# Kernel tuning notes

Measured on AMD Instinct MI355X. Metric: run time of the kernel, lower is better.

## Reference

```python
import jax, jax.numpy as jnp
import numpy as np

EPS = 1e-6

def _rms_norm(x, w):
    # per-head RMSNorm over last dim (head_dim)
    var = jnp.mean(jnp.square(x), axis=-1, keepdims=True)
    return x * jax.lax.rsqrt(var + EPS) * w

def _linear(x, w, b):
    # torch nn.Linear: y = x @ W^T + b
    return jnp.einsum('bsd,od->bso', x, w) + b

def setup_inputs() -> dict:
    key = jax.random.key(0)
    ks = jax.random.split(key, 16)
    B, S, S_enc, D, H, HD = 1, 2048, 256, 1536, 24, 64
    w = lambda k: jax.random.normal(k, (D, D), dtype=jnp.float32) * 0.02
    return {
        'hidden_states': jax.random.normal(ks[0], (B, S, D), dtype=jnp.float32),
        'encoder_hidden_states': jax.random.normal(ks[1], (B, S_enc, D), dtype=jnp.float32),
        'attention_mask': jnp.zeros((B, 1, 1, S + S_enc), dtype=jnp.float32),
        'to_q_weight': w(ks[2]), 'to_q_bias': jnp.zeros((D,), jnp.float32),
        'to_k_weight': w(ks[3]), 'to_k_bias': jnp.zeros((D,), jnp.float32),
        'to_v_weight': w(ks[4]), 'to_v_bias': jnp.zeros((D,), jnp.float32),
        'norm_q_weight': jnp.ones((HD,), jnp.float32),
        'norm_k_weight': jnp.ones((HD,), jnp.float32),
        'add_q_proj_weight': w(ks[5]), 'add_q_proj_bias': jnp.zeros((D,), jnp.float32),
        'add_k_proj_weight': w(ks[6]), 'add_k_proj_bias': jnp.zeros((D,), jnp.float32),
        'add_v_proj_weight': w(ks[7]), 'add_v_proj_bias': jnp.zeros((D,), jnp.float32),
        'norm_added_q_weight': jnp.ones((HD,), jnp.float32),
        'norm_added_k_weight': jnp.ones((HD,), jnp.float32),
        'to_out_0_weight': w(ks[8]), 'to_out_0_bias': jnp.zeros((D,), jnp.float32),
        'to_add_out_weight': w(ks[9]), 'to_add_out_bias': jnp.zeros((D,), jnp.float32),
        'attn_heads': 24,
        'attn_head_dim': 64,
    }

def reference(hidden_states, encoder_hidden_states, attention_mask,
              to_q_weight, to_q_bias, to_k_weight, to_k_bias, to_v_weight, to_v_bias,
              norm_q_weight, norm_k_weight,
              add_q_proj_weight, add_q_proj_bias, add_k_proj_weight, add_k_proj_bias,
              add_v_proj_weight, add_v_proj_bias,
              norm_added_q_weight, norm_added_k_weight,
              to_out_0_weight, to_out_0_bias, to_add_out_weight, to_add_out_bias,
              attn_heads, attn_head_dim):
    B, S, D = hidden_states.shape
    S_enc = encoder_hidden_states.shape[1]
    H, HD = attn_heads, attn_head_dim
    scale = float(HD) ** -0.5

    def split_heads(x):  # [B,T,H*HD] -> [B,H,T,HD]
        return x.reshape(B, -1, H, HD).transpose(0, 2, 1, 3)

    # hidden-stream QKV + per-head RMSNorm on q,k
    q = _rms_norm(split_heads(_linear(hidden_states, to_q_weight, to_q_bias)), norm_q_weight)
    k = _rms_norm(split_heads(_linear(hidden_states, to_k_weight, to_k_bias)), norm_k_weight)
    v = split_heads(_linear(hidden_states, to_v_weight, to_v_bias))

    # encoder-stream QKV + per-head RMSNorm on q,k
    eq = _rms_norm(split_heads(_linear(encoder_hidden_states, add_q_proj_weight, add_q_proj_bias)), norm_added_q_weight)
    ek = _rms_norm(split_heads(_linear(encoder_hidden_states, add_k_proj_weight, add_k_proj_bias)), norm_added_k_weight)
    ev = split_heads(_linear(encoder_hidden_states, add_v_proj_weight, add_v_proj_bias))

    # concat streams along sequence: [B,H,S+S_enc,HD]
    q = jnp.concatenate([q, eq], axis=2)
    k = jnp.concatenate([k, ek], axis=2)
    v = jnp.concatenate([v, ev], axis=2)

    # SDPA with additive mask
    scores = jnp.einsum('bhqd,bhkd->bhqk', q, k) * scale + attention_mask
    probs = jax.nn.softmax(scores, axis=-1)
    out = jnp.einsum('bhqk,bhkd->bhqd', probs, v)  # [B,H,T,HD]
    out = out.transpose(0, 2, 1, 3).reshape(B, S + S_enc, H * HD)

    # split back into image / text streams, separate output projections
    attn_output = _linear(out[:, :S], to_out_0_weight, to_out_0_bias)
    context_attn_output = _linear(out[:, S:], to_add_out_weight, to_add_out_bias)
    del context_attn_output  # AttentionFunc returns only the hidden-stream output
    return attn_output
```

## Files before the change

### kernel.cpp

```cpp
#include <hip/hip_runtime.h>
#include <cstdint>


typedef __attribute__((ext_vector_type(8))) short s16x8;
typedef __attribute__((ext_vector_type(4))) float f32x4;

#define LOG2E 1.4426950408889634f

__device__ __forceinline__ short f2bf(float f) {
  union { float f; uint32_t u; } v; v.f = f;
  uint32_t r = v.u + 0x7FFFu + ((v.u >> 16) & 1u);
  return (short)(r >> 16);
}
__device__ __forceinline__ short f2bf_fast(float f) {
  union { float f; uint32_t u; } v; v.f = f;
  return (short)((v.u + 0x8000u) >> 16);
}

typedef uint32_t __attribute__((address_space(1)))* gas_u32;
typedef uint32_t __attribute__((address_space(3)))* las_u32;

__device__ __forceinline__ void gload_lds16(const short* g, short* l) {
  __builtin_amdgcn_global_load_lds((gas_u32)(g), (las_u32)(l), 16, 0, 0);
}

struct CvtSeg { const float* src; short* dst; int n4; };
struct CvtArgs { CvtSeg s[8]; };

__global__ __launch_bounds__(256) void cvt_bf16_kernel(CvtArgs a) {
  const int stride = gridDim.x * blockDim.x;
  const int tid = blockIdx.x * blockDim.x + threadIdx.x;
  for (int i = 0; i < 8; ++i) {
    const float4* src = (const float4*)a.s[i].src;
    short* dst = a.s[i].dst;
    const int n4 = a.s[i].n4;
    for (int j = tid; j < n4; j += stride) {
      float4 v = src[j];
      short4 o;
      o.x = f2bf(v.x); o.y = f2bf(v.y); o.z = f2bf(v.z); o.w = f2bf(v.w);
      *(short4*)(dst + (size_t)j * 4) = o;
    }
  }
}

enum { MODE_Q = 0, MODE_K = 1, MODE_V = 2, MODE_OUT = 3 };

struct GemmCfg {
  const short* A;
  const short* W;
  const float* bias;
  const float* normw;
  void* dst;
  int toff;
  int mode;
  int mtiles;
};
struct GemmArgs { GemmCfg c[5]; };

__global__ __launch_bounds__(256) void proj_gemm_kernel(GemmArgs args) {
  const GemmCfg cfg = args.c[blockIdx.z];
  if ((int)blockIdx.y >= cfg.mtiles) return;
  constexpr int K = 1536;
  __shared__ short As[8192];
  __shared__ short Bs[8192];
  const int t = threadIdx.x;
  const int lane = t & 63;
  const int wave = t >> 6;
  const int l16 = lane & 15;
  const int quad = lane >> 4;
  const int wm = wave >> 1;
  const int wn = wave & 1;

  const short* __restrict__ Ag = cfg.A + (size_t)(blockIdx.y * 128) * K;
  const short* __restrict__ Wg = cfg.W + (size_t)(blockIdx.x * 128) * K;
  const int srow = t >> 3;
  const int cpos = t & 7;
  const int srcc = cpos ^ (srow & 7);

  const f32x4 z4 = {0.f, 0.f, 0.f, 0.f};
  f32x4 acc[4][4];
#pragma unroll
  for (int i = 0; i < 4; ++i) {
#pragma unroll
    for (int j = 0; j < 4; ++j) acc[i][j] = z4;
  }

  for (int k0 = 0; k0 < K; k0 += 64) {
#pragma unroll
    for (int j = 0; j < 4; ++j) {
      const size_t roff = (size_t)(j * 32 + srow) * K + k0 + srcc * 8;
      gload_lds16(Ag + roff, As + j * 2048 + t * 8);
      gload_lds16(Wg + roff, Bs + j * 2048 + t * 8);
    }
    __syncthreads();
#pragma unroll
    for (int kh = 0; kh < 2; ++kh) {
      s16x8 af[4], bfr[4];
#pragma unroll
      for (int i = 0; i < 4; ++i) {
        int pos = (kh * 4 + quad) ^ (l16 & 7);
        af[i]  = *(const s16x8*)(As + (wm * 64 + i * 16 + l16) * 64 + pos * 8);
        bfr[i] = *(const s16x8*)(Bs + (wn * 64 + i * 16 + l16) * 64 + pos * 8);
      }
#pragma unroll
      for (int mi = 0; mi < 4; ++mi) {
#pragma unroll
        for (int ni = 0; ni < 4; ++ni)
          acc[mi][ni] = __builtin_amdgcn_mfma_f32_16x16x32_bf16(af[mi], bfr[ni], acc[mi][ni], 0, 0, 0);
      }
    }
    __syncthreads();
  }

  const int nbase = blockIdx.x * 128 + wn * 64;
  const int mbase = blockIdx.y * 128 + wm * 64;
  const int mode = cfg.mode;
  const int h = nbase >> 6;

  float biasv[4], nwv[4];
#pragma unroll
  for (int ni = 0; ni < 4; ++ni) {
    int col = nbase + ni * 16 + l16;
    biasv[ni] = cfg.bias[col];
    nwv[ni] = (mode == MODE_Q || mode == MODE_K) ? cfg.normw[col & 63] : 0.f;
  }

#pragma unroll
  for (int mi = 0; mi < 4; ++mi) {
    float vv[4][4];
#pragma unroll
    for (int ni = 0; ni < 4; ++ni) {
#pragma unroll
      for (int r = 0; r < 4; ++r) vv[ni][r] = acc[mi][ni][r] + biasv[ni];
    }
    if (mode == MODE_Q || mode == MODE_K) {
      float ss[4];
#pragma unroll
      for (int r = 0; r < 4; ++r)
        ss[r] = vv[0][r] * vv[0][r] + vv[1][r] * vv[1][r] +
                vv[2][r] * vv[2][r] + vv[3][r] * vv[3][r];
#pragma unroll
      for (int r = 0; r < 4; ++r) {
        ss[r] += __shfl_xor(ss[r], 1);
        ss[r] += __shfl_xor(ss[r], 2);
        ss[r] += __shfl_xor(ss[r], 4);
        ss[r] += __shfl_xor(ss[r], 8);
        float rs = rsqrtf(ss[r] * (1.0f / 64.0f) + 1e-6f);
#pragma unroll
        for (int ni = 0; ni < 4; ++ni) vv[ni][r] *= rs * nwv[ni];
      }
    }
    const int row0 = mbase + mi * 16 + quad * 4;
    if (mode == MODE_Q) {
      short* Qd = (short*)cfg.dst;
#pragma unroll
      for (int ni = 0; ni < 4; ++ni) {
        int d = ni * 16 + l16;
#pragma unroll
        for (int r = 0; r < 4; ++r)
          Qd[((size_t)h * 2048 + row0 + r) * 64 + d] = f2bf(vv[ni][r]);
      }
    } else if (mode == MODE_K) {
      short* Kd = (short*)cfg.dst;
#pragma unroll
      for (int ni = 0; ni < 4; ++ni) {
        int d = ni * 16 + l16;
#pragma unroll
        for (int r = 0; r < 4; ++r)
          Kd[((size_t)h * 2304 + cfg.toff + row0 + r) * 64 + d] = f2bf(vv[ni][r]);
      }
    } else if (mode == MODE_V) {
      short* Vd = (short*)cfg.dst;
#pragma unroll
      for (int ni = 0; ni < 4; ++ni) {
        int d = ni * 16 + l16;
        short4 o4;
        o4.x = f2bf(vv[ni][0]); o4.y = f2bf(vv[ni][1]);
        o4.z = f2bf(vv[ni][2]); o4.w = f2bf(vv[ni][3]);
        *(short4*)(Vd + ((size_t)h * 64 + d) * 2304 + cfg.toff + row0) = o4;
      }
    } else {
      float* Od = (float*)cfg.dst;
#pragma unroll
      for (int ni = 0; ni < 4; ++ni) {
        int col = nbase + ni * 16 + l16;
#pragma unroll
        for (int r = 0; r < 4; ++r)
          Od[(size_t)(row0 + r) * 1536 + col] = vv[ni][r];
      }
    }
  }
}

__global__ __launch_bounds__(256) void flash_kernel(
    const short* __restrict__ Q, const short* __restrict__ Kc,
    const short* __restrict__ VT, const float* __restrict__ mask,
    short* __restrict__ AO) {
  const int b = blockIdx.x;
  const int h = (b & 7) * 3 + ((b >> 3) % 3);
  const int q0 = ((b >> 3) / 3) * 32;
  const int lane = threadIdx.x & 63;
  const int wave = threadIdx.x >> 6;
  const int qw = wave & 1;
  const int ks = wave >> 1;
  const int l16 = lane & 15;
  const int quad = lane >> 4;

  __shared__ __align__(16) short smem[18432];
  short* Pw = smem + 16384 + wave * 512;

  const short* Kh = Kc + (size_t)h * 2304 * 64;
  const short* Vh = VT + (size_t)h * 64 * 2304;

  const short* Qrow = Q + ((size_t)h * 2048 + q0 + qw * 16 + l16) * 64;
  s16x8 aq0 = *(const s16x8*)(Qrow + quad * 8);
  s16x8 aq1 = *(const s16x8*)(Qrow + quad * 8 + 32);

  s16x8 ones;
#pragma unroll
  for (int i = 0; i < 8; ++i) ones[i] = (short)0x3F80;

  const f32x4 z4 = {0.f, 0.f, 0.f, 0.f};
  f32x4 o[4] = {z4, z4, z4, z4};
  f32x4 lacc = z4;
  const float SC = 0.125f * LOG2E;
  const int kbase = ks * 1152;

  auto stage = [&](int it, int buf) {
    const int kb = kbase + it * 32;
    short* kt = smem + (ks * 2 + buf) * 2048;
    short* vt = smem + 8192 + (ks * 2 + buf) * 2048;
#pragma unroll
    for (int c = 0; c < 2; ++c) {
      int s = c * 128 + qw * 64 + lane;
      int trow = s >> 3, cp = s & 7;
      gload_lds16(Kh + (size_t)(kb + trow) * 64 + (cp ^ (trow & 7)) * 8,
                  kt + c * 1024 + qw * 512 + lane * 8);
      int d = s >> 2, cpv = s & 3;
      gload_lds16(Vh + (size_t)d * 2304 + kb + ((cpv ^ ((d >> 1) & 3)) * 8),
                  vt + c * 1024 + qw * 512 + lane * 8);
    }
  };

  stage(0, 0);
  __syncthreads();

  for (int it = 0; it < 36; ++it) {
    const int buf = it & 1;
    if (it < 35) stage(it + 1, buf ^ 1);
    const short* kt = smem + (ks * 2 + buf) * 2048;
    const short* vt = smem + 8192 + (ks * 2 + buf) * 2048;
    const int kb = kbase + it * 32;

#pragma unroll
    for (int ni = 0; ni < 2; ++ni) {
      const int tt = ni * 16 + l16;
      const short* kr = kt + tt * 64;
      s16x8 bk0 = *(const s16x8*)(kr + ((quad ^ (tt & 7)) << 3));
      s16x8 bk1 = *(const s16x8*)(kr + (((quad + 4) ^ (tt & 7)) << 3));
      f32x4 p0 = __builtin_amdgcn_mfma_f32_16x16x32_bf16(aq0, bk0, z4, 0, 0, 0);
      f32x4 s  = __builtin_amdgcn_mfma_f32_16x16x32_bf16(aq1, bk1, p0, 0, 0, 0);
      float mvl = mask[kb + tt] * LOG2E;
      const int cc = tt >> 3;
#pragma unroll
      for (int rr = 0; rr < 4; ++rr) {
        float pv = __builtin_amdgcn_exp2f(fmaf(s[rr], SC, mvl));
        int prow = quad * 4 + rr;
        Pw[prow * 32 + ((cc ^ ((prow >> 1) & 3)) << 3) + (tt & 7)] = f2bf_fast(pv);
      }
    }
    s16x8 ap = *(const s16x8*)(Pw + l16 * 32 + ((quad ^ ((l16 >> 1) & 3)) << 3));
    lacc = __builtin_amdgcn_mfma_f32_16x16x32_bf16(ap, ones, lacc, 0, 0, 0);
#pragma unroll
    for (int ni = 0; ni < 4; ++ni) {
      const int d = ni * 16 + l16;
      s16x8 bv = *(const s16x8*)(vt + d * 32 + ((quad ^ ((d >> 1) & 3)) << 3));
      o[ni] = __builtin_amdgcn_mfma_f32_16x16x32_bf16(ap, bv, o[ni], 0, 0, 0);
    }
    __syncthreads();
  }

  f32x4* R = (f32x4*)smem;
  if (ks == 1) {
    f32x4* Rw = R + (qw * 64 + lane) * 5;
#pragma unroll
    for (int ni = 0; ni < 4; ++ni) Rw[ni] = o[ni];
    Rw[4] = lacc;
  }
  __syncthreads();
  if (ks == 0) {
    const f32x4* Rw = R + (qw * 64 + lane) * 5;
#pragma unroll
    for (int ni = 0; ni < 4; ++ni) o[ni] += Rw[ni];
    lacc += Rw[4];
#pragma unroll
    for (int rr = 0; rr < 4; ++rr) {
      float inv = 1.0f / lacc[rr];
      int tq = q0 + qw * 16 + quad * 4 + rr;
#pragma unroll
      for (int ni = 0; ni < 4; ++ni)
        AO[(size_t)tq * 1536 + h * 64 + ni * 16 + l16] = f2bf(o[ni][rr] * inv);
    }
  }
}

extern "C" void kernel_launch(void* const* d_in, const int* in_sizes, int n_in,
                              void* d_out, int out_size, void* d_ws, size_t ws_size,
                              hipStream_t stream) {
  (void)in_sizes; (void)n_in; (void)out_size; (void)ws_size;
  const float* hidden = (const float*)d_in[0];
  const float* enc    = (const float*)d_in[1];
  const float* amask  = (const float*)d_in[2];
  const float* wq  = (const float*)d_in[3];  const float* bq  = (const float*)d_in[4];
  const float* wk  = (const float*)d_in[5];  const float* bk  = (const float*)d_in[6];
  const float* wv  = (const float*)d_in[7];  const float* bv  = (const float*)d_in[8];
  const float* nqw = (const float*)d_in[9];  const float* nkw = (const float*)d_in[10];
  const float* wak = (const float*)d_in[13]; const float* bak = (const float*)d_in[14];
  const float* wav = (const float*)d_in[15]; const float* bav = (const float*)d_in[16];
  const float* nakw = (const float*)d_in[18];
  const float* wo  = (const float*)d_in[19]; const float* bo  = (const float*)d_in[20];
  float* out = (float*)d_out;

  char* p = (char*)d_ws;
  auto carve = [&](size_t bytes) { char* r = p; p += (bytes + 255) & ~(size_t)255; return r; };
  short* Xb   = (short*)carve((size_t)2048 * 1536 * 2);
  short* Eb   = (short*)carve((size_t)256 * 1536 * 2);
  short* Wqb  = (short*)carve((size_t)1536 * 1536 * 2);
  short* Wkb  = (short*)carve((size_t)1536 * 1536 * 2);
  short* Wvb  = (short*)carve((size_t)1536 * 1536 * 2);
  short* Wakb = (short*)carve((size_t)1536 * 1536 * 2);
  short* Wavb = (short*)carve((size_t)1536 * 1536 * 2);
  short* Wob  = (short*)carve((size_t)1536 * 1536 * 2);
  short* Qb   = (short*)carve((size_t)24 * 2048 * 64 * 2);
  short* Kb   = (short*)carve((size_t)24 * 2304 * 64 * 2);
  short* VTb  = (short*)carve((size_t)24 * 64 * 2304 * 2);
  short* AOb  = (short*)carve((size_t)2048 * 1536 * 2);

  CvtArgs ca;
  ca.s[0] = {hidden, Xb, 2048 * 1536 / 4};
  ca.s[1] = {enc,    Eb, 256 * 1536 / 4};
  ca.s[2] = {wq,  Wqb,  1536 * 1536 / 4};
  ca.s[3] = {wk,  Wkb,  1536 * 1536 / 4};
  ca.s[4] = {wv,  Wvb,  1536 * 1536 / 4};
  ca.s[5] = {wak, Wakb, 1536 * 1536 / 4};
  ca.s[6] = {wav, Wavb, 1536 * 1536 / 4};
  ca.s[7] = {wo,  Wob,  1536 * 1536 / 4};
  cvt_bf16_kernel<<<dim3(1024), dim3(256), 0, stream>>>(ca);

  GemmArgs g1;
  g1.c[0] = {Xb, Wqb,  bq,  nqw,     (void*)Qb,  0,    MODE_Q, 16};
  g1.c[1] = {Xb, Wkb,  bk,  nkw,     (void*)Kb,  0,    MODE_K, 16};
  g1.c[2] = {Xb, Wvb,  bv,  nullptr, (void*)VTb, 0,    MODE_V, 16};
  g1.c[3] = {Eb, Wakb, bak, nakw,    (void*)Kb,  2048, MODE_K, 2};
  g1.c[4] = {Eb, Wavb, bav, nullptr, (void*)VTb, 2048, MODE_V, 2};
  proj_gemm_kernel<<<dim3(12, 16, 5), dim3(256), 0, stream>>>(g1);

  flash_kernel<<<dim3(1536), dim3(256), 0, stream>>>(Qb, Kb, VTb, amask, AOb);

  GemmArgs g3;
  g3.c[0] = {AOb, Wob, bo, nullptr, (void*)out, 0, MODE_OUT, 16};
  proj_gemm_kernel<<<dim3(12, 16, 1), dim3(256), 0, stream>>>(g3);
}
```

Baseline: 325.6 us.

## Double query rows per flash block and shrink GEMM K-step to 32

```diff
diff --git a/kernel.cpp b/kernel.cpp
--- a/kernel.cpp
+++ b/kernel.cpp
@@ -61,8 +61,8 @@
   const GemmCfg cfg = args.c[blockIdx.z];
   if ((int)blockIdx.y >= cfg.mtiles) return;
   constexpr int K = 1536;
-  __shared__ short As[8192];
-  __shared__ short Bs[8192];
+  __shared__ short As[4096];
+  __shared__ short Bs[4096];
   const int t = threadIdx.x;
   const int lane = t & 63;
   const int wave = t >> 6;
@@ -73,9 +73,8 @@
 
   const short* __restrict__ Ag = cfg.A + (size_t)(blockIdx.y * 128) * K;
   const short* __restrict__ Wg = cfg.W + (size_t)(blockIdx.x * 128) * K;
-  const int srow = t >> 3;
-  const int cpos = t & 7;
-  const int srcc = cpos ^ (srow & 7);
+  const int srow = t >> 2;
+  const int scol = (t & 3) << 3;
 
   const f32x4 z4 = {0.f, 0.f, 0.f, 0.f};
   f32x4 acc[4][4];
@@ -85,29 +84,24 @@
     for (int j = 0; j < 4; ++j) acc[i][j] = z4;
   }
 
-  for (int k0 = 0; k0 < K; k0 += 64) {
-#pragma unroll
-    for (int j = 0; j < 4; ++j) {
-      const size_t roff = (size_t)(j * 32 + srow) * K + k0 + srcc * 8;
-      gload_lds16(Ag + roff, As + j * 2048 + t * 8);
-      gload_lds16(Wg + roff, Bs + j * 2048 + t * 8);
-    }
+  for (int k0 = 0; k0 < K; k0 += 32) {
+    gload_lds16(Ag + (size_t)srow * K + k0 + scol, As + t * 8);
+    gload_lds16(Ag + (size_t)(srow + 64) * K + k0 + scol, As + 2048 + t * 8);
+    gload_lds16(Wg + (size_t)srow * K + k0 + scol, Bs + t * 8);
+    gload_lds16(Wg + (size_t)(srow + 64) * K + k0 + scol, Bs + 2048 + t * 8);
     __syncthreads();
-#pragma unroll
-    for (int kh = 0; kh < 2; ++kh) {
-      s16x8 af[4], bfr[4];
-#pragma unroll
-      for (int i = 0; i < 4; ++i) {
-        int pos = (kh * 4 + quad) ^ (l16 & 7);
-        af[i]  = *(const s16x8*)(As + (wm * 64 + i * 16 + l16) * 64 + pos * 8);
-        bfr[i] = *(const s16x8*)(Bs + (wn * 64 + i * 16 + l16) * 64 + pos * 8);
-      }
-#pragma unroll
-      for (int mi = 0; mi < 4; ++mi) {
-#pragma unroll
-        for (int ni = 0; ni < 4; ++ni)
-          acc[mi][ni] = __builtin_amdgcn_mfma_f32_16x16x32_bf16(af[mi], bfr[ni], acc[mi][ni], 0, 0, 0);
-      }
+    s16x8 af[4], bfr[4];
+#pragma unroll
+    for (int i = 0; i < 4; ++i)
+      af[i] = *(const s16x8*)(As + (wm * 64 + i * 16 + l16) * 32 + quad * 8);
+#pragma unroll
+    for (int i = 0; i < 4; ++i)
+      bfr[i] = *(const s16x8*)(Bs + (wn * 64 + i * 16 + l16) * 32 + quad * 8);
+#pragma unroll
+    for (int mi = 0; mi < 4; ++mi) {
+#pragma unroll
+      for (int ni = 0; ni < 4; ++ni)
+        acc[mi][ni] = __builtin_amdgcn_mfma_f32_16x16x32_bf16(af[mi], bfr[ni], acc[mi][ni], 0, 0, 0);
     }
     __syncthreads();
   }
@@ -198,7 +192,7 @@
     short* __restrict__ AO) {
   const int b = blockIdx.x;
   const int h = (b & 7) * 3 + ((b >> 3) % 3);
-  const int q0 = ((b >> 3) / 3) * 32;
+  const int q0 = ((b >> 3) / 3) * 64;
   const int lane = threadIdx.x & 63;
   const int wave = threadIdx.x >> 6;
   const int qw = wave & 1;
@@ -206,23 +200,31 @@
   const int l16 = lane & 15;
   const int quad = lane >> 4;
 
-  __shared__ __align__(16) short smem[18432];
-  short* Pw = smem + 16384 + wave * 512;
+  __shared__ __align__(16) short smem[20480];
 
   const short* Kh = Kc + (size_t)h * 2304 * 64;
   const short* Vh = VT + (size_t)h * 64 * 2304;
 
-  const short* Qrow = Q + ((size_t)h * 2048 + q0 + qw * 16 + l16) * 64;
-  s16x8 aq0 = *(const s16x8*)(Qrow + quad * 8);
-  s16x8 aq1 = *(const s16x8*)(Qrow + quad * 8 + 32);
+  s16x8 aq0[2], aq1[2];
+#pragma unroll
+  for (int g = 0; g < 2; ++g) {
+    const short* Qrow =
+        Q + ((size_t)h * 2048 + q0 + qw * 32 + g * 16 + l16) * 64;
+    aq0[g] = *(const s16x8*)(Qrow + quad * 8);
+    aq1[g] = *(const s16x8*)(Qrow + quad * 8 + 32);
+  }
 
   s16x8 ones;
 #pragma unroll
   for (int i = 0; i < 8; ++i) ones[i] = (short)0x3F80;
 
   const f32x4 z4 = {0.f, 0.f, 0.f, 0.f};
-  f32x4 o[4] = {z4, z4, z4, z4};
-  f32x4 lacc = z4;
+  f32x4 o[2][4];
+#pragma unroll
+  for (int g = 0; g < 2; ++g)
+#pragma unroll
+    for (int ni = 0; ni < 4; ++ni) o[g][ni] = z4;
+  f32x4 lacc[2] = {z4, z4};
   const float SC = 0.125f * LOG2E;
   const int kbase = ks * 1152;
 
@@ -232,12 +234,12 @@
     short* vt = smem + 8192 + (ks * 2 + buf) * 2048;
 #pragma unroll
     for (int c = 0; c < 2; ++c) {
-      int s = c * 128 + qw * 64 + lane;
-      int trow = s >> 3, cp = s & 7;
-      gload_lds16(Kh + (size_t)(kb + trow) * 64 + (cp ^ (trow & 7)) * 8,
+      const int gi = c * 128 + qw * 64 + lane;
+      const int trow = gi >> 3, cp = gi & 7;
+      gload_lds16(Kh + (size_t)(kb + trow) * 64 + ((cp ^ (trow & 7)) << 3),
                   kt + c * 1024 + qw * 512 + lane * 8);
-      int d = s >> 2, cpv = s & 3;
-      gload_lds16(Vh + (size_t)d * 2304 + kb + ((cpv ^ ((d >> 1) & 3)) * 8),
+      const int d = gi >> 2, cpv = gi & 3;
+      gload_lds16(Vh + (size_t)d * 2304 + kb + ((cpv ^ ((d >> 1) & 3)) << 3),
                   vt + c * 1024 + qw * 512 + lane * 8);
     }
   };
@@ -252,54 +254,75 @@
     const short* vt = smem + 8192 + (ks * 2 + buf) * 2048;
     const int kb = kbase + it * 32;
 
+    s16x8 bk[2][2];
 #pragma unroll
     for (int ni = 0; ni < 2; ++ni) {
       const int tt = ni * 16 + l16;
       const short* kr = kt + tt * 64;
-      s16x8 bk0 = *(const s16x8*)(kr + ((quad ^ (tt & 7)) << 3));
-      s16x8 bk1 = *(const s16x8*)(kr + (((quad + 4) ^ (tt & 7)) << 3));
-      f32x4 p0 = __builtin_amdgcn_mfma_f32_16x16x32_bf16(aq0, bk0, z4, 0, 0, 0);
-      f32x4 s  = __builtin_amdgcn_mfma_f32_16x16x32_bf16(aq1, bk1, p0, 0, 0, 0);
-      float mvl = mask[kb + tt] * LOG2E;
-      const int cc = tt >> 3;
-#pragma unroll
-      for (int rr = 0; rr < 4; ++rr) {
-        float pv = __builtin_amdgcn_exp2f(fmaf(s[rr], SC, mvl));
-        int prow = quad * 4 + rr;
-        Pw[prow * 32 + ((cc ^ ((prow >> 1) & 3)) << 3) + (tt & 7)] = f2bf_fast(pv);
-      }
-    }
-    s16x8 ap = *(const s16x8*)(Pw + l16 * 32 + ((quad ^ ((l16 >> 1) & 3)) << 3));
-    lacc = __builtin_amdgcn_mfma_f32_16x16x32_bf16(ap, ones, lacc, 0, 0, 0);
+      bk[ni][0] = *(const s16x8*)(kr + ((quad ^ (tt & 7)) << 3));
+      bk[ni][1] = *(const s16x8*)(kr + (((quad + 4) ^ (tt & 7)) << 3));
+    }
+    s16x8 bv[4];
 #pragma unroll
     for (int ni = 0; ni < 4; ++ni) {
       const int d = ni * 16 + l16;
-      s16x8 bv = *(const s16x8*)(vt + d * 32 + ((quad ^ ((d >> 1) & 3)) << 3));
-      o[ni] = __builtin_amdgcn_mfma_f32_16x16x32_bf16(ap, bv, o[ni], 0, 0, 0);
+      bv[ni] = *(const s16x8*)(vt + d * 32 + ((quad ^ ((d >> 1) & 3)) << 3));
+    }
+    float mvl[2];
+#pragma unroll
+    for (int ni = 0; ni < 2; ++ni) mvl[ni] = mask[kb + ni * 16 + l16] * LOG2E;
+
+#pragma unroll
+    for (int g = 0; g < 2; ++g) {
+      short* Pg = smem + 16384 + wave * 1024 + g * 512;
+#pragma unroll
+      for (int ni = 0; ni < 2; ++ni) {
+        f32x4 s = __builtin_amdgcn_mfma_f32_16x16x32_bf16(aq0[g], bk[ni][0], z4, 0, 0, 0);
+        s = __builtin_amdgcn_mfma_f32_16x16x32_bf16(aq1[g], bk[ni][1], s, 0, 0, 0);
+        const int tt = ni * 16 + l16;
+        const int cc = tt >> 3;
+#pragma unroll
+        for (int rr = 0; rr < 4; ++rr) {
+          float pv = __builtin_amdgcn_exp2f(fmaf(s[rr], SC, mvl[ni]));
+          const int prow = quad * 4 + rr;
+          Pg[prow * 32 + ((cc ^ ((prow >> 1) & 3)) << 3) + (tt & 7)] = f2bf_fast(pv);
+        }
+      }
+      s16x8 ap = *(const s16x8*)(Pg + l16 * 32 + ((quad ^ ((l16 >> 1) & 3)) << 3));
+      lacc[g] = __builtin_amdgcn_mfma_f32_16x16x32_bf16(ap, ones, lacc[g], 0, 0, 0);
+#pragma unroll
+      for (int ni = 0; ni < 4; ++ni)
+        o[g][ni] = __builtin_amdgcn_mfma_f32_16x16x32_bf16(ap, bv[ni], o[g][ni], 0, 0, 0);
     }
     __syncthreads();
   }
 
   f32x4* R = (f32x4*)smem;
   if (ks == 1) {
-    f32x4* Rw = R + (qw * 64 + lane) * 5;
-#pragma unroll
-    for (int ni = 0; ni < 4; ++ni) Rw[ni] = o[ni];
-    Rw[4] = lacc;
+    f32x4* Rw = R + (qw * 64 + lane) * 10;
+#pragma unroll
+    for (int g = 0; g < 2; ++g) {
+#pragma unroll
+      for (int ni = 0; ni < 4; ++ni) Rw[g * 5 + ni] = o[g][ni];
+      Rw[g * 5 + 4] = lacc[g];
+    }
   }
   __syncthreads();
   if (ks == 0) {
-    const f32x4* Rw = R + (qw * 64 + lane) * 5;
-#pragma unroll
-    for (int ni = 0; ni < 4; ++ni) o[ni] += Rw[ni];
-    lacc += Rw[4];
-#pragma unroll
-    for (int rr = 0; rr < 4; ++rr) {
-      float inv = 1.0f / lacc[rr];
-      int tq = q0 + qw * 16 + quad * 4 + rr;
-#pragma unroll
-      for (int ni = 0; ni < 4; ++ni)
-        AO[(size_t)tq * 1536 + h * 64 + ni * 16 + l16] = f2bf(o[ni][rr] * inv);
+    const f32x4* Rw = R + (qw * 64 + lane) * 10;
+#pragma unroll
+    for (int g = 0; g < 2; ++g) {
+#pragma unroll
+      for (int ni = 0; ni < 4; ++ni) o[g][ni] += Rw[g * 5 + ni];
+      f32x4 ls = lacc[g] + Rw[g * 5 + 4];
+#pragma unroll
+      for (int rr = 0; rr < 4; ++rr) {
+        float inv = 1.0f / ls[rr];
+        int tq = q0 + qw * 32 + g * 16 + quad * 4 + rr;
+#pragma unroll
+        for (int ni = 0; ni < 4; ++ni)
+          AO[(size_t)tq * 1536 + h * 64 + ni * 16 + l16] = f2bf(o[g][ni][rr] * inv);
+      }
     }
   }
 }
@@ -355,7 +378,7 @@
   g1.c[4] = {Eb, Wavb, bav, nullptr, (void*)VTb, 2048, MODE_V, 2};
   proj_gemm_kernel<<<dim3(12, 16, 5), dim3(256), 0, stream>>>(g1);
 
-  flash_kernel<<<dim3(1536), dim3(256), 0, stream>>>(Qb, Kb, VTb, amask, AOb);
+  flash_kernel<<<dim3(768), dim3(256), 0, stream>>>(Qb, Kb, VTb, amask, AOb);
 
   GemmArgs g3;
   g3.c[0] = {AOb, Wob, bo, nullptr, (void*)out, 0, MODE_OUT, 16};
```

Result: faster. 292.5 us (-10.2%).
